# Optimization experiments

Hardware: AMD Instinct MI355X
Metric: run time of the kernel (lower is better)

Reference implementation:

```python
import jax, jax.numpy as jnp
import numpy as np

D_MODEL = 1024
NHEAD = 16
HEAD_DIM = D_MODEL // NHEAD  # 64
Q_STRIDE = 2
KV_STRIDE = 1
ROPE_BASE = 10000.0


def _rope_tables(positions):
    # positions: [L] int -> cos/sin [L, HEAD_DIM]
    half = HEAD_DIM // 2
    inv_freq = 1.0 / (ROPE_BASE ** (jnp.arange(half, dtype=jnp.float32) / half))
    freqs = positions.astype(jnp.float32)[:, None] * inv_freq[None, :]  # [L, half]
    emb = jnp.concatenate([freqs, freqs], axis=-1)  # [L, HEAD_DIM]
    return jnp.cos(emb), jnp.sin(emb)


def _rotate_half(x):
    half = x.shape[-1] // 2
    return jnp.concatenate([-x[..., half:], x[..., :half]], axis=-1)


def _apply_rope(x, cos, sin):
    # x: [B, H, L, D]; cos/sin: [L, D] broadcast over B, H
    return x * cos + _rotate_half(x) * sin


def setup_inputs() -> dict:
    key = jax.random.key(0)
    ks = jax.random.split(key, 10)
    B, S, K = 4, 1024, 2048
    s = 0.02
    return {
        "query": jax.random.normal(ks[0], (B, S, D_MODEL), jnp.float32),
        "kv": jax.random.normal(ks[1], (B, K, D_MODEL), jnp.float32),
        "q_w": jax.random.normal(ks[2], (D_MODEL, D_MODEL), jnp.float32) * s,
        "q_b": jax.random.normal(ks[3], (D_MODEL,), jnp.float32) * s,
        "k_w": jax.random.normal(ks[4], (D_MODEL, D_MODEL), jnp.float32) * s,
        "k_b": jax.random.normal(ks[5], (D_MODEL,), jnp.float32) * s,
        "v_w": jax.random.normal(ks[6], (D_MODEL, D_MODEL), jnp.float32) * s,
        "v_b": jax.random.normal(ks[7], (D_MODEL,), jnp.float32) * s,
        "out_w": jax.random.normal(ks[8], (D_MODEL, D_MODEL), jnp.float32) * s,
        "out_b": jax.random.normal(ks[9], (D_MODEL,), jnp.float32) * s,
    }


def reference(query, kv, q_w, q_b, k_w, k_b, v_w, v_b, out_w, out_b):
    B, S, _ = query.shape
    K = kv.shape[1]
    # Projections (torch Linear: x @ W^T + b), reshape to [B, H, L, D]
    q = (query @ q_w.T + q_b).reshape(B, S, NHEAD, HEAD_DIM).transpose(0, 2, 1, 3)
    k = (kv @ k_w.T + k_b).reshape(B, K, NHEAD, HEAD_DIM).transpose(0, 2, 1, 3)
    v = (kv @ v_w.T + v_b).reshape(B, K, NHEAD, HEAD_DIM).transpose(0, 2, 1, 3)
    # RoPE at strided original frame positions
    q_cos, q_sin = _rope_tables(jnp.arange(S) * Q_STRIDE)
    k_cos, k_sin = _rope_tables(jnp.arange(K) * KV_STRIDE)
    q = _apply_rope(q, q_cos, q_sin)
    k = _apply_rope(k, k_cos, k_sin)
    scale = 1.0 / np.sqrt(HEAD_DIM).astype(np.float32)
    attn = jnp.einsum('bhsd,bhkd->bhsk', q, k) * scale  # [B, H, S, K]
    attn = jax.nn.softmax(attn, axis=-1)
    out = jnp.einsum('bhsk,bhkd->bhsd', attn, v)
    out = out.transpose(0, 2, 1, 3).reshape(B, S, D_MODEL)
    return out @ out_w.T + out_b
```

## Files before the change

kernel.cpp:

```cpp
#include <hip/hip_runtime.h>
#include <hip/hip_bf16.h>

#define D_MODEL 1024
#define NHEAD   16
#define HD      64
#define SQ      1024
#define SK      2048

typedef __attribute__((ext_vector_type(8))) short bh8;
typedef __attribute__((ext_vector_type(4))) float fx4;

#define QSCALE 0.1803368801111204f

__device__ __forceinline__ unsigned short f2bf(float f) {
  union { float f; unsigned u; } v; v.f = f;
  return (unsigned short)((v.u + 0x7FFFu + ((v.u >> 16) & 1u)) >> 16);
}

__device__ __forceinline__ float bf2f(unsigned short u) {
  union { unsigned u; float f; } v; v.u = ((unsigned)u) << 16; return v.f;
}

#define GLOAD_LDS16(gp, lp)                                                  \
  __builtin_amdgcn_global_load_lds(                                         \
      (const __attribute__((address_space(1))) unsigned int*)(gp),          \
      (__attribute__((address_space(3))) unsigned int*)(lp), 16, 0, 0)

__global__ __launch_bounds__(256) void cvt_kernel(
    const float* __restrict__ q, const float* __restrict__ kv,
    const float* __restrict__ qw, const float* __restrict__ kw,
    const float* __restrict__ vw, const float* __restrict__ ow,
    unsigned short* __restrict__ qx, unsigned short* __restrict__ kvx,
    unsigned short* __restrict__ qwx, unsigned short* __restrict__ kwx,
    unsigned short* __restrict__ vwx, unsigned short* __restrict__ owx)
{
  const int idx = blockIdx.x * 256 + threadIdx.x;
  const float* src; unsigned short* dst; size_t off;
  if (idx < 524288)        { src = q;  dst = qx;  off = idx; }
  else if (idx < 1572864)  { src = kv; dst = kvx; off = idx - 524288; }
  else {
    const int w = idx - 1572864; const int sel = w >> 17; off = w & 131071;
    src = sel == 0 ? qw : sel == 1 ? kw : sel == 2 ? vw : ow;
    dst = sel == 0 ? qwx : sel == 1 ? kwx : sel == 2 ? vwx : owx;
  }
  const float4 a = ((const float4*)src)[off * 2];
  const float4 b = ((const float4*)src)[off * 2 + 1];
  bh8 r;
  r[0] = (short)f2bf(a.x); r[1] = (short)f2bf(a.y);
  r[2] = (short)f2bf(a.z); r[3] = (short)f2bf(a.w);
  r[4] = (short)f2bf(b.x); r[5] = (short)f2bf(b.y);
  r[6] = (short)f2bf(b.z); r[7] = (short)f2bf(b.w);
  *(bh8*)(dst + off * 8) = r;
}

__global__ __launch_bounds__(256) void qkv_kernel(
    const unsigned short* __restrict__ qx, const unsigned short* __restrict__ kvx,
    const unsigned short* __restrict__ qw, const unsigned short* __restrict__ kw,
    const unsigned short* __restrict__ vw,
    const float* __restrict__ qb, const float* __restrict__ kb,
    const float* __restrict__ vb,
    unsigned short* __restrict__ outq, unsigned short* __restrict__ outk,
    unsigned short* __restrict__ outv)
{
  __shared__ unsigned short Alds[8192];
  __shared__ unsigned short Blds[8192];

  const int t = threadIdx.x;
  const int lane = t & 63, w = t >> 6;
  const int lr = lane & 15, g = lane >> 4;
  const int bid = blockIdx.x;
  const bool isQ = bid >= 1024;
  int bx, by;
  if (isQ) { const int tq = bid - 1024; bx = tq & 7; by = tq >> 3; }
  else     { bx = bid & 15; by = bid >> 4; }
  const int row0 = by * 128;
  const int colB = bx * 128;
  const int wrow = (w >> 1) * 64;
  const int wcol = (w & 1) * 64;

  const unsigned short* X = isQ ? qx : kvx;
  const unsigned short* Wsrc; const float* bias; int colW; bool isK = false;
  if (isQ)              { Wsrc = qw; bias = qb; colW = colB; }
  else if (colB < 1024) { Wsrc = kw; bias = kb; colW = colB; isK = true; }
  else                  { Wsrc = vw; bias = vb; colW = colB - 1024; }

  const int rbase = t >> 3;
  const int sw8 = (((t & 7) ^ (rbase & 7))) * 8;

  const int sl0 = ((g) ^ (lr & 7)) * 8;
  const int sl1 = ((4 + g) ^ (lr & 7)) * 8;

  fx4 acc[4][4] = {};
  for (int k0 = 0; k0 < 1024; k0 += 64) {
    __syncthreads();
#pragma unroll
    for (int l = 0; l < 4; ++l)
      GLOAD_LDS16(X + (size_t)(row0 + rbase + l * 32) * 1024 + k0 + sw8,
                  &Alds[l * 2048 + t * 8]);
#pragma unroll
    for (int l = 0; l < 4; ++l)
      GLOAD_LDS16(Wsrc + (size_t)(colW + rbase + l * 32) * 1024 + k0 + sw8,
                  &Blds[l * 2048 + t * 8]);
    __syncthreads();

#pragma unroll
    for (int kk = 0; kk < 2; ++kk) {
      const int sl = kk ? sl1 : sl0;
      bh8 af[4], bf[4];
#pragma unroll
      for (int mi = 0; mi < 4; ++mi)
        af[mi] = *(const bh8*)&Alds[(wrow + mi * 16 + lr) * 64 + sl];
#pragma unroll
      for (int ni = 0; ni < 4; ++ni)
        bf[ni] = *(const bh8*)&Blds[(wcol + ni * 16 + lr) * 64 + sl];
      __builtin_amdgcn_s_setprio(1);
#pragma unroll
      for (int mi = 0; mi < 4; ++mi)
#pragma unroll
        for (int ni = 0; ni < 4; ++ni)
          acc[mi][ni] = __builtin_amdgcn_mfma_f32_16x16x32_bf16(af[mi], bf[ni], acc[mi][ni], 0, 0, 0);
      __builtin_amdgcn_s_setprio(0);
    }
  }

  float bv[4];
#pragma unroll
  for (int ni = 0; ni < 4; ++ni) bv[ni] = bias[colW + wcol + ni * 16 + lr];
#pragma unroll
  for (int mi = 0; mi < 4; ++mi)
#pragma unroll
    for (int ni = 0; ni < 4; ++ni)
#pragma unroll
      for (int j = 0; j < 4; ++j) acc[mi][ni][j] += bv[ni];

  const int LMASK = isQ ? 1023 : 2047;
  if (isQ || isK) {
    const float c0 = 0.41524101186092029f;
    const float invf0 = exp2f(-(float)lr * c0);
    const float invf1 = exp2f(-(float)(16 + lr) * c0);
#pragma unroll
    for (int mi = 0; mi < 4; ++mi)
#pragma unroll
      for (int j = 0; j < 4; ++j) {
        const int rg = row0 + wrow + mi * 16 + 4 * g + j;
        const int s = rg & LMASK;
        const float pos = (float)(isQ ? 2 * s : s);
#pragma unroll
        for (int ni = 0; ni < 2; ++ni) {
          float sn, cs;
          __sincosf(pos * (ni == 0 ? invf0 : invf1), &sn, &cs);
          const float x1 = acc[mi][ni][j], x2 = acc[mi][ni + 2][j];
          acc[mi][ni][j]     = x1 * cs - x2 * sn;
          acc[mi][ni + 2][j] = x2 * cs + x1 * sn;
        }
      }
  }

  const int h = (colW + wcol) >> 6;
#pragma unroll
  for (int mi = 0; mi < 4; ++mi)
#pragma unroll
    for (int j = 0; j < 4; ++j) {
      const int rg = row0 + wrow + mi * 16 + 4 * g + j;
      const int bb = isQ ? (rg >> 10) : (rg >> 11);
      const int s = rg & LMASK;
#pragma unroll
      for (int ni = 0; ni < 4; ++ni) {
        const int d = ni * 16 + lr;
        if (isQ) {
          outq[(((size_t)(bb * 16 + h)) * SQ + s) * 64 + d] = f2bf(acc[mi][ni][j] * QSCALE);
        } else {
          const size_t base = ((size_t)(bb * 16 + h)) * (SK * 64);
          if (isK)
            outk[base + (s >> 4) * 1024 + (d >> 5) * 512 + ((d >> 3) & 3) * 128 + (s & 15) * 8 + (d & 7)]
                = f2bf(acc[mi][ni][j]);
          else
            outv[base + (s >> 5) * 2048 + (d >> 4) * 512 + ((s >> 3) & 3) * 128 + (d & 15) * 8 + (s & 7)]
                = f2bf(acc[mi][ni][j]);
        }
      }
    }
}

__global__ __launch_bounds__(256) void oproj_kernel(
    const unsigned short* __restrict__ A, const unsigned short* __restrict__ W,
    const float* __restrict__ bias, float* __restrict__ out)
{
  __shared__ unsigned short Alds[4096];
  __shared__ unsigned short Blds[8192];

  const int t = threadIdx.x;
  const int lane = t & 63, w = t >> 6;
  const int lr = lane & 15, g = lane >> 4;
  const int bid = blockIdx.x;
  const int bx = bid & 7, by = bid >> 3;
  const int row0 = by * 64;
  const int colB = bx * 128;
  const int wrow = (w >> 1) * 32;
  const int wcol = (w & 1) * 64;

  const int rbase = t >> 3;
  const int sw8 = (((t & 7) ^ (rbase & 7))) * 8;
  const int sl0 = ((g) ^ (lr & 7)) * 8;
  const int sl1 = ((4 + g) ^ (lr & 7)) * 8;

  fx4 acc[2][4] = {};
  for (int k0 = 0; k0 < 1024; k0 += 64) {
    __syncthreads();
#pragma unroll
    for (int l = 0; l < 2; ++l)
      GLOAD_LDS16(A + (size_t)(row0 + rbase + l * 32) * 1024 + k0 + sw8,
                  &Alds[l * 2048 + t * 8]);
#pragma unroll
    for (int l = 0; l < 4; ++l)
      GLOAD_LDS16(W + (size_t)(colB + rbase + l * 32) * 1024 + k0 + sw8,
                  &Blds[l * 2048 + t * 8]);
    __syncthreads();

#pragma unroll
    for (int kk = 0; kk < 2; ++kk) {
      const int sl = kk ? sl1 : sl0;
      bh8 af[2], bf[4];
#pragma unroll
      for (int mi = 0; mi < 2; ++mi)
        af[mi] = *(const bh8*)&Alds[(wrow + mi * 16 + lr) * 64 + sl];
#pragma unroll
      for (int ni = 0; ni < 4; ++ni)
        bf[ni] = *(const bh8*)&Blds[(wcol + ni * 16 + lr) * 64 + sl];
      __builtin_amdgcn_s_setprio(1);
#pragma unroll
      for (int mi = 0; mi < 2; ++mi)
#pragma unroll
        for (int ni = 0; ni < 4; ++ni)
          acc[mi][ni] = __builtin_amdgcn_mfma_f32_16x16x32_bf16(af[mi], bf[ni], acc[mi][ni], 0, 0, 0);
      __builtin_amdgcn_s_setprio(0);
    }
  }

  float bv[4];
#pragma unroll
  for (int ni = 0; ni < 4; ++ni) bv[ni] = bias[colB + wcol + ni * 16 + lr];
#pragma unroll
  for (int mi = 0; mi < 2; ++mi)
#pragma unroll
    for (int j = 0; j < 4; ++j) {
      const int rg = row0 + wrow + mi * 16 + 4 * g + j;
#pragma unroll
      for (int ni = 0; ni < 4; ++ni)
        out[(size_t)rg * 1024 + colB + wcol + ni * 16 + lr] = acc[mi][ni][j] + bv[ni];
    }
}

__global__ __launch_bounds__(256, 4) void attn_kernel(
    const unsigned short* __restrict__ Qr, const unsigned short* __restrict__ Kt,
    const unsigned short* __restrict__ Vt, unsigned short* __restrict__ O)
{
  __shared__ __align__(16) unsigned short smem[4 * 2304];
  __shared__ float llds[4][32];

  const int lane = threadIdx.x & 63;
  const int w = threadIdx.x >> 6;
  const int lr = lane & 15, g = lane >> 4, kl = g * 8;
  const int bid = blockIdx.x;
  const int swz = (bid & 7) * 256 + (bid >> 3);
  const int bh = swz >> 5;
  const int q0 = (swz & 31) * 32;
  const int b = bh >> 4, h = bh & 15;

  unsigned short* p_lds = smem + w * 2304;

  const unsigned short* Qp = Qr + (size_t)bh * SQ * HD;
  const unsigned short* Kp = Kt + (size_t)bh * SK * HD;
  const unsigned short* Vp = Vt + (size_t)bh * SK * HD;

  bh8 qf[2][2];
#pragma unroll
  for (int mi = 0; mi < 2; ++mi)
#pragma unroll
    for (int kk = 0; kk < 2; ++kk)
      qf[mi][kk] = *(const bh8*)(Qp + (size_t)(q0 + mi * 16 + lr) * 64 + kk * 32 + kl);

  bh8 ones;
#pragma unroll
  for (int i = 0; i < 8; ++i) ones[i] = (short)0x3F80;

  fx4 oacc[2][4] = {};
  fx4 lacc[2] = {};

  for (int t = 0; t < 8; ++t) {
    fx4 sacc[2][4] = {};
#pragma unroll
    for (int kk = 0; kk < 2; ++kk) {
      bh8 kf[4];
#pragma unroll
      for (int ni = 0; ni < 4; ++ni)
        kf[ni] = *(const bh8*)(Kp + (size_t)(w * 32 + t * 4 + ni) * 1024 + kk * 512 + g * 128 + lr * 8);
      __builtin_amdgcn_s_setprio(1);
#pragma unroll
      for (int mi = 0; mi < 2; ++mi)
#pragma unroll
        for (int ni = 0; ni < 4; ++ni)
          sacc[mi][ni] = __builtin_amdgcn_mfma_f32_16x16x32_bf16(qf[mi][kk], kf[ni], sacc[mi][ni], 0, 0, 0);
      __builtin_amdgcn_s_setprio(0);
    }

    asm volatile("s_waitcnt lgkmcnt(0)" ::: "memory");
    __builtin_amdgcn_sched_barrier(0);

#pragma unroll
    for (int mi = 0; mi < 2; ++mi)
#pragma unroll
      for (int ni = 0; ni < 4; ++ni) {
        float p0, p1, p2, p3;
        asm("v_exp_f32 %0, %1" : "=v"(p0) : "v"(sacc[mi][ni][0]));
        asm("v_exp_f32 %0, %1" : "=v"(p1) : "v"(sacc[mi][ni][1]));
        asm("v_exp_f32 %0, %1" : "=v"(p2) : "v"(sacc[mi][ni][2]));
        asm("v_exp_f32 %0, %1" : "=v"(p3) : "v"(sacc[mi][ni][3]));
        unsigned lo, hi;
        asm("v_cvt_pk_bf16_f32 %0, %1, %2" : "=v"(lo) : "v"(p0), "v"(p1));
        asm("v_cvt_pk_bf16_f32 %0, %1, %2" : "=v"(hi) : "v"(p2), "v"(p3));
        unsigned short* base = &p_lds[(mi * 16 + 4 * g) * 68 + ni * 16 + lr];
        base[0]   = (unsigned short)lo;
        base[68]  = (unsigned short)(lo >> 16);
        base[136] = (unsigned short)hi;
        base[204] = (unsigned short)(hi >> 16);
      }

    asm volatile("s_waitcnt lgkmcnt(0)" ::: "memory");
    __builtin_amdgcn_sched_barrier(0);

#pragma unroll
    for (int kk = 0; kk < 2; ++kk) {
      bh8 pa[2], vb[4];
#pragma unroll
      for (int mi = 0; mi < 2; ++mi) {
        const unsigned short* pp = &p_lds[(mi * 16 + lr) * 68 + kk * 32 + kl];
        const short4 a = *(const short4*)pp;
        const short4 c = *(const short4*)(pp + 4);
        pa[mi][0] = a.x; pa[mi][1] = a.y; pa[mi][2] = a.z; pa[mi][3] = a.w;
        pa[mi][4] = c.x; pa[mi][5] = c.y; pa[mi][6] = c.z; pa[mi][7] = c.w;
      }
#pragma unroll
      for (int ni = 0; ni < 4; ++ni)
        vb[ni] = *(const bh8*)(Vp + (size_t)(w * 16 + t * 2 + kk) * 2048 + ni * 512 + g * 128 + lr * 8);
      __builtin_amdgcn_s_setprio(1);
#pragma unroll
      for (int mi = 0; mi < 2; ++mi) {
#pragma unroll
        for (int ni = 0; ni < 4; ++ni)
          oacc[mi][ni] = __builtin_amdgcn_mfma_f32_16x16x32_bf16(pa[mi], vb[ni], oacc[mi][ni], 0, 0, 0);
        lacc[mi] = __builtin_amdgcn_mfma_f32_16x16x32_bf16(pa[mi], ones, lacc[mi], 0, 0, 0);
      }
      __builtin_amdgcn_s_setprio(0);
    }
  }

  if (lr == 0) {
#pragma unroll
    for (int mi = 0; mi < 2; ++mi)
#pragma unroll
      for (int j = 0; j < 4; ++j)
        llds[w][mi * 16 + 4 * g + j] = lacc[mi][j];
  }

  asm volatile("s_waitcnt lgkmcnt(0)" ::: "memory");
  __builtin_amdgcn_sched_barrier(0);
  unsigned short* opart = smem + w * 2304;
#pragma unroll
  for (int mi = 0; mi < 2; ++mi)
#pragma unroll
    for (int j = 0; j < 4; ++j) {
      const int row = mi * 16 + 4 * g + j;
#pragma unroll
      for (int ni = 0; ni < 4; ++ni)
        opart[row * 72 + ni * 16 + lr] = f2bf(oacc[mi][ni][j]);
    }
  __syncthreads();

  const int row = threadIdx.x >> 3;
  const int d0 = (threadIdx.x & 7) * 8;
  float a8[8] = {};
#pragma unroll
  for (int ww = 0; ww < 4; ++ww) {
    const bh8 v = *(const bh8*)(smem + ww * 2304 + row * 72 + d0);
#pragma unroll
    for (int i = 0; i < 8; ++i) a8[i] += bf2f((unsigned short)v[i]);
  }
  const float inv = 1.0f / (llds[0][row] + llds[1][row] + llds[2][row] + llds[3][row]);
  bh8 r;
#pragma unroll
  for (int i = 0; i < 8; ++i) r[i] = (short)f2bf(a8[i] * inv);
  *(bh8*)&O[((size_t)(b * SQ + q0 + row)) * D_MODEL + h * 64 + d0] = r;
}

extern "C" void kernel_launch(void* const* d_in, const int* in_sizes, int n_in,
                              void* d_out, int out_size, void* d_ws, size_t ws_size,
                              hipStream_t stream) {
  (void)in_sizes; (void)n_in; (void)out_size; (void)ws_size;
  const float* query = (const float*)d_in[0];
  const float* kv    = (const float*)d_in[1];
  const float* q_w   = (const float*)d_in[2];
  const float* q_b   = (const float*)d_in[3];
  const float* k_w   = (const float*)d_in[4];
  const float* k_b   = (const float*)d_in[5];
  const float* v_w   = (const float*)d_in[6];
  const float* v_b   = (const float*)d_in[7];
  const float* out_w = (const float*)d_in[8];
  const float* out_b = (const float*)d_in[9];
  float* out = (float*)d_out;

  unsigned short* ws = (unsigned short*)d_ws;
  unsigned short* qx     = ws;
  unsigned short* kvx    = ws + ((size_t)4  << 20);
  unsigned short* qwx    = ws + ((size_t)12 << 20);
  unsigned short* kwx    = ws + ((size_t)13 << 20);
  unsigned short* vwx    = ws + ((size_t)14 << 20);
  unsigned short* owx    = ws + ((size_t)15 << 20);
  unsigned short* q_rope = ws + ((size_t)16 << 20);
  unsigned short* k_t    = ws + ((size_t)20 << 20);
  unsigned short* v_t    = ws + ((size_t)28 << 20);
  unsigned short* attn_o = qx;

  hipLaunchKernelGGL(cvt_kernel, dim3(8192), dim3(256), 0, stream,
                     query, kv, q_w, k_w, v_w, out_w, qx, kvx, qwx, kwx, vwx, owx);
  hipLaunchKernelGGL(qkv_kernel, dim3(1280), dim3(256), 0, stream,
                     qx, kvx, qwx, kwx, vwx, q_b, k_b, v_b, q_rope, k_t, v_t);
  hipLaunchKernelGGL(attn_kernel, dim3(2048), dim3(256), 0, stream,
                     q_rope, k_t, v_t, attn_o);
  hipLaunchKernelGGL(oproj_kernel, dim3(512), dim3(256), 0, stream,
                     attn_o, owx, out_b, out);
}
```

Measured before the change: 158.7 us.

## Replace LDS-staged GEMM tiles with direct global loads in projection kernels

Both the QKV projection and output projection kernels drop the shared-memory staging and barriers, so each wave loads its A and B fragments straight from global memory into registers. Blocks are regrouped so the four waves share one 64-row A strip and each wave owns its own 64 columns. The output projection moves to 64x256 block tiles with half as many blocks. This removes LDS traffic and syncs, but each wave now fetches its own operands with no reuse across waves except through cache, and global load latency is exposed inside the MFMA loop.

```diff
diff --git a/kernel.cpp b/kernel.cpp
--- a/kernel.cpp
+++ b/kernel.cpp
@@ -20,11 +20,6 @@
 __device__ __forceinline__ float bf2f(unsigned short u) {
   union { unsigned u; float f; } v; v.u = ((unsigned)u) << 16; return v.f;
 }
-
-#define GLOAD_LDS16(gp, lp)                                                  \
-  __builtin_amdgcn_global_load_lds(                                         \
-      (const __attribute__((address_space(1))) unsigned int*)(gp),          \
-      (__attribute__((address_space(3))) unsigned int*)(lp), 16, 0, 0)
 
 __global__ __launch_bounds__(256) void cvt_kernel(
     const float* __restrict__ q, const float* __restrict__ kv,
@@ -53,7 +48,7 @@
   *(bh8*)(dst + off * 8) = r;
 }
 
-__global__ __launch_bounds__(256) void qkv_kernel(
+__global__ __launch_bounds__(256, 3) void qkv_kernel(
     const unsigned short* __restrict__ qx, const unsigned short* __restrict__ kvx,
     const unsigned short* __restrict__ qw, const unsigned short* __restrict__ kw,
     const unsigned short* __restrict__ vw,
@@ -62,57 +57,43 @@
     unsigned short* __restrict__ outq, unsigned short* __restrict__ outk,
     unsigned short* __restrict__ outv)
 {
-  __shared__ unsigned short Alds[8192];
-  __shared__ unsigned short Blds[8192];
-
   const int t = threadIdx.x;
   const int lane = t & 63, w = t >> 6;
   const int lr = lane & 15, g = lane >> 4;
   const int bid = blockIdx.x;
   const bool isQ = bid >= 1024;
-  int bx, by;
-  if (isQ) { const int tq = bid - 1024; bx = tq & 7; by = tq >> 3; }
-  else     { bx = bid & 15; by = bid >> 4; }
-  const int row0 = by * 128;
-  const int colB = bx * 128;
-  const int wrow = (w >> 1) * 64;
-  const int wcol = (w & 1) * 64;
+  int rowblk, ngrp;
+  if (isQ) { const int tq = bid - 1024; ngrp = tq & 3; rowblk = tq >> 2; }
+  else     { ngrp = bid & 7; rowblk = bid >> 3; }
+  const int row0 = rowblk * 64;
+  const int c0 = ngrp * 256 + w * 64;
 
   const unsigned short* X = isQ ? qx : kvx;
-  const unsigned short* Wsrc; const float* bias; int colW; bool isK = false;
-  if (isQ)              { Wsrc = qw; bias = qb; colW = colB; }
-  else if (colB < 1024) { Wsrc = kw; bias = kb; colW = colB; isK = true; }
-  else                  { Wsrc = vw; bias = vb; colW = colB - 1024; }
-
-  const int rbase = t >> 3;
-  const int sw8 = (((t & 7) ^ (rbase & 7))) * 8;
-
-  const int sl0 = ((g) ^ (lr & 7)) * 8;
-  const int sl1 = ((4 + g) ^ (lr & 7)) * 8;
+  const unsigned short* Wsrc; const float* bias; int cW; bool isK = false;
+  if (isQ)            { Wsrc = qw; bias = qb; cW = c0; }
+  else if (c0 < 1024) { Wsrc = kw; bias = kb; cW = c0; isK = true; }
+  else                { Wsrc = vw; bias = vb; cW = c0 - 1024; }
+
+  const unsigned short* ap[4];
+  const unsigned short* bp[4];
+#pragma unroll
+  for (int mi = 0; mi < 4; ++mi)
+    ap[mi] = X + (size_t)(row0 + mi * 16 + lr) * 1024 + g * 8;
+#pragma unroll
+  for (int ni = 0; ni < 4; ++ni)
+    bp[ni] = Wsrc + (size_t)(cW + ni * 16 + lr) * 1024 + g * 8;
 
   fx4 acc[4][4] = {};
   for (int k0 = 0; k0 < 1024; k0 += 64) {
-    __syncthreads();
-#pragma unroll
-    for (int l = 0; l < 4; ++l)
-      GLOAD_LDS16(X + (size_t)(row0 + rbase + l * 32) * 1024 + k0 + sw8,
-                  &Alds[l * 2048 + t * 8]);
-#pragma unroll
-    for (int l = 0; l < 4; ++l)
-      GLOAD_LDS16(Wsrc + (size_t)(colW + rbase + l * 32) * 1024 + k0 + sw8,
-                  &Blds[l * 2048 + t * 8]);
-    __syncthreads();
-
 #pragma unroll
     for (int kk = 0; kk < 2; ++kk) {
-      const int sl = kk ? sl1 : sl0;
       bh8 af[4], bf[4];
 #pragma unroll
       for (int mi = 0; mi < 4; ++mi)
-        af[mi] = *(const bh8*)&Alds[(wrow + mi * 16 + lr) * 64 + sl];
-#pragma unroll
-      for (int ni = 0; ni < 4; ++ni)
-        bf[ni] = *(const bh8*)&Blds[(wcol + ni * 16 + lr) * 64 + sl];
+        af[mi] = *(const bh8*)(ap[mi] + k0 + kk * 32);
+#pragma unroll
+      for (int ni = 0; ni < 4; ++ni)
+        bf[ni] = *(const bh8*)(bp[ni] + k0 + kk * 32);
       __builtin_amdgcn_s_setprio(1);
 #pragma unroll
       for (int mi = 0; mi < 4; ++mi)
@@ -125,7 +106,7 @@
 
   float bv[4];
 #pragma unroll
-  for (int ni = 0; ni < 4; ++ni) bv[ni] = bias[colW + wcol + ni * 16 + lr];
+  for (int ni = 0; ni < 4; ++ni) bv[ni] = bias[cW + ni * 16 + lr];
 #pragma unroll
   for (int mi = 0; mi < 4; ++mi)
 #pragma unroll
@@ -135,14 +116,14 @@
 
   const int LMASK = isQ ? 1023 : 2047;
   if (isQ || isK) {
-    const float c0 = 0.41524101186092029f;
-    const float invf0 = exp2f(-(float)lr * c0);
-    const float invf1 = exp2f(-(float)(16 + lr) * c0);
+    const float c0f = 0.41524101186092029f;
+    const float invf0 = exp2f(-(float)lr * c0f);
+    const float invf1 = exp2f(-(float)(16 + lr) * c0f);
 #pragma unroll
     for (int mi = 0; mi < 4; ++mi)
 #pragma unroll
       for (int j = 0; j < 4; ++j) {
-        const int rg = row0 + wrow + mi * 16 + 4 * g + j;
+        const int rg = row0 + mi * 16 + 4 * g + j;
         const int s = rg & LMASK;
         const float pos = (float)(isQ ? 2 * s : s);
 #pragma unroll
@@ -156,12 +137,12 @@
       }
   }
 
-  const int h = (colW + wcol) >> 6;
+  const int h = cW >> 6;
 #pragma unroll
   for (int mi = 0; mi < 4; ++mi)
 #pragma unroll
     for (int j = 0; j < 4; ++j) {
-      const int rg = row0 + wrow + mi * 16 + 4 * g + j;
+      const int rg = row0 + mi * 16 + 4 * g + j;
       const int bb = isQ ? (rg >> 10) : (rg >> 11);
       const int s = rg & LMASK;
 #pragma unroll
@@ -182,54 +163,41 @@
     }
 }
 
-__global__ __launch_bounds__(256) void oproj_kernel(
+__global__ __launch_bounds__(256, 3) void oproj_kernel(
     const unsigned short* __restrict__ A, const unsigned short* __restrict__ W,
     const float* __restrict__ bias, float* __restrict__ out)
 {
-  __shared__ unsigned short Alds[4096];
-  __shared__ unsigned short Blds[8192];
-
   const int t = threadIdx.x;
   const int lane = t & 63, w = t >> 6;
   const int lr = lane & 15, g = lane >> 4;
   const int bid = blockIdx.x;
-  const int bx = bid & 7, by = bid >> 3;
-  const int row0 = by * 64;
-  const int colB = bx * 128;
-  const int wrow = (w >> 1) * 32;
-  const int wcol = (w & 1) * 64;
-
-  const int rbase = t >> 3;
-  const int sw8 = (((t & 7) ^ (rbase & 7))) * 8;
-  const int sl0 = ((g) ^ (lr & 7)) * 8;
-  const int sl1 = ((4 + g) ^ (lr & 7)) * 8;
-
-  fx4 acc[2][4] = {};
+  const int ngrp = bid & 3, rowblk = bid >> 2;
+  const int row0 = rowblk * 64;
+  const int c0 = ngrp * 256 + w * 64;
+
+  const unsigned short* ap[4];
+  const unsigned short* bp[4];
+#pragma unroll
+  for (int mi = 0; mi < 4; ++mi)
+    ap[mi] = A + (size_t)(row0 + mi * 16 + lr) * 1024 + g * 8;
+#pragma unroll
+  for (int ni = 0; ni < 4; ++ni)
+    bp[ni] = W + (size_t)(c0 + ni * 16 + lr) * 1024 + g * 8;
+
+  fx4 acc[4][4] = {};
   for (int k0 = 0; k0 < 1024; k0 += 64) {
-    __syncthreads();
-#pragma unroll
-    for (int l = 0; l < 2; ++l)
-      GLOAD_LDS16(A + (size_t)(row0 + rbase + l * 32) * 1024 + k0 + sw8,
-                  &Alds[l * 2048 + t * 8]);
-#pragma unroll
-    for (int l = 0; l < 4; ++l)
-      GLOAD_LDS16(W + (size_t)(colB + rbase + l * 32) * 1024 + k0 + sw8,
-                  &Blds[l * 2048 + t * 8]);
-    __syncthreads();
-
 #pragma unroll
     for (int kk = 0; kk < 2; ++kk) {
-      const int sl = kk ? sl1 : sl0;
-      bh8 af[2], bf[4];
-#pragma unroll
-      for (int mi = 0; mi < 2; ++mi)
-        af[mi] = *(const bh8*)&Alds[(wrow + mi * 16 + lr) * 64 + sl];
-#pragma unroll
-      for (int ni = 0; ni < 4; ++ni)
-        bf[ni] = *(const bh8*)&Blds[(wcol + ni * 16 + lr) * 64 + sl];
+      bh8 af[4], bf[4];
+#pragma unroll
+      for (int mi = 0; mi < 4; ++mi)
+        af[mi] = *(const bh8*)(ap[mi] + k0 + kk * 32);
+#pragma unroll
+      for (int ni = 0; ni < 4; ++ni)
+        bf[ni] = *(const bh8*)(bp[ni] + k0 + kk * 32);
       __builtin_amdgcn_s_setprio(1);
 #pragma unroll
-      for (int mi = 0; mi < 2; ++mi)
+      for (int mi = 0; mi < 4; ++mi)
 #pragma unroll
         for (int ni = 0; ni < 4; ++ni)
           acc[mi][ni] = __builtin_amdgcn_mfma_f32_16x16x32_bf16(af[mi], bf[ni], acc[mi][ni], 0, 0, 0);
@@ -239,15 +207,15 @@
 
   float bv[4];
 #pragma unroll
-  for (int ni = 0; ni < 4; ++ni) bv[ni] = bias[colB + wcol + ni * 16 + lr];
-#pragma unroll
-  for (int mi = 0; mi < 2; ++mi)
+  for (int ni = 0; ni < 4; ++ni) bv[ni] = bias[c0 + ni * 16 + lr];
+#pragma unroll
+  for (int mi = 0; mi < 4; ++mi)
 #pragma unroll
     for (int j = 0; j < 4; ++j) {
-      const int rg = row0 + wrow + mi * 16 + 4 * g + j;
-#pragma unroll
-      for (int ni = 0; ni < 4; ++ni)
-        out[(size_t)rg * 1024 + colB + wcol + ni * 16 + lr] = acc[mi][ni][j] + bv[ni];
+      const int rg = row0 + mi * 16 + 4 * g + j;
+#pragma unroll
+      for (int ni = 0; ni < 4; ++ni)
+        out[(size_t)rg * 1024 + c0 + ni * 16 + lr] = acc[mi][ni][j] + bv[ni];
     }
 }
 
@@ -427,6 +395,6 @@
                      qx, kvx, qwx, kwx, vwx, q_b, k_b, v_b, q_rope, k_t, v_t);
   hipLaunchKernelGGL(attn_kernel, dim3(2048), dim3(256), 0, stream,
                      q_rope, k_t, v_t, attn_o);
-  hipLaunchKernelGGL(oproj_kernel, dim3(512), dim3(256), 0, stream,
+  hipLaunchKernelGGL(oproj_kernel, dim3(256), dim3(256), 0, stream,
                      attn_o, owx, out_b, out);
 }
```

New measurement: 249.5 us. 57.2% more time.
